# Optimization experiments

Hardware: AMD Instinct MI355X
Metric: run time of the kernel (lower is better)

## Reference

```python
import jax, jax.numpy as jnp
import numpy as np

B, T, D, H, O, E = 4, 2048, 1024, 2048, 1024, 8
EPS = 1e-12  # torch F.normalize p=1 eps


def setup_inputs() -> dict:
    key = jax.random.key(0)
    ks = jax.random.split(key, 8)
    s = lambda *dims: 1.0 / np.sqrt(dims[0])
    return {
        "x": jax.random.normal(ks[0], (B, T, D), dtype=jnp.float32),
        "num_experts_chosen": 2,
        "W_gate": jax.random.normal(ks[1], (D, E), dtype=jnp.float32) * s(D),
        "b_gate": jnp.zeros((E,), dtype=jnp.float32),
        "W1": jax.random.normal(ks[2], (E, D, H), dtype=jnp.float32) * s(D),
        "b1": jnp.zeros((E, H), dtype=jnp.float32),
        "W2": jax.random.normal(ks[3], (E, H, O), dtype=jnp.float32) * s(H),
        "b2": jnp.zeros((E, O), dtype=jnp.float32),
    }


def reference(x, num_experts_chosen, W_gate, b_gate, W1, b1, W2, b2):
    # Router: softmax over experts -> [b, t, E]
    gating = jax.nn.softmax(jnp.einsum("btd,de->bte", x, W_gate) + b_gate, axis=-1)

    # Top-k mask (scatter of ones at top-k indices), then L1 renormalize
    _, topk_idx = jax.lax.top_k(gating, num_experts_chosen)  # [b, t, k]
    mask = jax.nn.one_hot(topk_idx, E, dtype=gating.dtype).sum(axis=-2)  # [b, t, E]
    g = gating * mask
    g = g / jnp.maximum(jnp.sum(jnp.abs(g), axis=-1, keepdims=True), EPS)

    # Dense compute of ALL experts (faithful to original), eval-mode dropout = identity
    h = jax.nn.relu(jnp.einsum("btd,edh->bteh", x, W1) + b1)  # [b, t, E, H]
    eo = jnp.einsum("bteh,eho->bteo", h, W2) + b2              # [b, t, E, O]

    # Weighted combine over experts
    return jnp.einsum("bte,bteo->bto", g, eo)
```

## Files before the change

kernel.cpp:

```cpp
#include <hip/hip_runtime.h>
#include <hip/hip_bf16.h>

typedef unsigned short u16;
typedef __attribute__((ext_vector_type(8))) short short8;
typedef __attribute__((ext_vector_type(4))) float floatx4;

#define NB 4
#define NT 2048
#define ND 1024
#define NH 2048
#define NO 1024
#define NE 8
#define NTOK (NB * NT)

#define BM2 256
#define BN2 256
#define BK2 32
#define BUFU (BM2 * BK2)

__device__ __forceinline__ u16 f2bf(float f) {
  __hip_bfloat16 h = __float2bfloat16(f);
  return *reinterpret_cast<u16*>(&h);
}

__device__ __forceinline__ float bf2f(unsigned u) {
  return __uint_as_float(u << 16);
}

__device__ __forceinline__ void async16(const u16* g, u16* l) {
  __builtin_amdgcn_global_load_lds(
      (const __attribute__((address_space(1))) void*)g,
      (__attribute__((address_space(3))) void*)l, 16, 0, 0);
}

__global__ __launch_bounds__(256) void transpose_cvt(
    const float* __restrict__ in, u16* __restrict__ out, int R, int C) {
  __shared__ float tile[64][65];
  int e = blockIdx.z;
  in  += (size_t)e * R * C;
  out += (size_t)e * R * C;
  int c0 = blockIdx.x * 64, r0 = blockIdx.y * 64;
  int t = threadIdx.x;
#pragma unroll
  for (int i = 0; i < 4; ++i) {
    int idx = t + i * 256;
    int r = idx >> 4, cq = idx & 15;
    float4 v = *(const float4*)&in[(size_t)(r0 + r) * C + c0 + cq * 4];
    tile[r][cq * 4 + 0] = v.x; tile[r][cq * 4 + 1] = v.y;
    tile[r][cq * 4 + 2] = v.z; tile[r][cq * 4 + 3] = v.w;
  }
  __syncthreads();
#pragma unroll
  for (int i = 0; i < 4; ++i) {
    int idx = t + i * 256;
    int c = idx >> 4, rq = idx & 15;
    uint2 p;
    p.x = (unsigned)f2bf(tile[rq * 4 + 0][c]) | ((unsigned)f2bf(tile[rq * 4 + 1][c]) << 16);
    p.y = (unsigned)f2bf(tile[rq * 4 + 2][c]) | ((unsigned)f2bf(tile[rq * 4 + 3][c]) << 16);
    *(uint2*)&out[(size_t)(c0 + c) * R + r0 + rq * 4] = p;
  }
}

__global__ __launch_bounds__(256) void router_kernel(
    const float* __restrict__ x, const float* __restrict__ Wg,
    const float* __restrict__ bg, u16* __restrict__ xbf,
    int* __restrict__ counts, int* __restrict__ entries,
    float* __restrict__ wts) {
  __shared__ int   se0[32], se1[32];
  __shared__ float sw0[32], sw1[32];
  int t = threadIdx.x;
  int tl = t >> 3;
  int l8 = t & 7;
  int tok = blockIdx.x * 32 + tl;

  const float* xrow = x + (size_t)tok * ND;
  u16* xbrow = xbf + (size_t)tok * ND;
  float acc[8] = {};
#pragma unroll 4
  for (int i = 0; i < 32; ++i) {
    int d0 = l8 * 4 + i * 32;
    float4 xv = *(const float4*)&xrow[d0];
    uint2 p;
    p.x = (unsigned)f2bf(xv.x) | ((unsigned)f2bf(xv.y) << 16);
    p.y = (unsigned)f2bf(xv.z) | ((unsigned)f2bf(xv.w) << 16);
    *(uint2*)&xbrow[d0] = p;
    const float* wr = Wg + (size_t)d0 * NE;
#pragma unroll
    for (int j = 0; j < 4; ++j) {
      float xs = (j == 0) ? xv.x : (j == 1) ? xv.y : (j == 2) ? xv.z : xv.w;
      float4 w0 = *(const float4*)&wr[j * NE];
      float4 w1 = *(const float4*)&wr[j * NE + 4];
      acc[0] += xs * w0.x; acc[1] += xs * w0.y;
      acc[2] += xs * w0.z; acc[3] += xs * w0.w;
      acc[4] += xs * w1.x; acc[5] += xs * w1.y;
      acc[6] += xs * w1.z; acc[7] += xs * w1.w;
    }
  }
#pragma unroll
  for (int off = 4; off; off >>= 1)
#pragma unroll
    for (int k = 0; k < 8; ++k) acc[k] += __shfl_down(acc[k], off, 8);

  if (l8 == 0) {
    float best = -1e30f, second = -1e30f;
    int e0 = 0, e1 = 0;
#pragma unroll
    for (int i = 0; i < NE; ++i) {
      float L = acc[i] + bg[i];
      if (L > best) { second = best; e1 = e0; best = L; e0 = i; }
      else if (L > second) { second = L; e1 = i; }
    }
    float p1 = __expf(second - best);
    float inv = 1.f / (1.f + p1);
    se0[tl] = e0; se1[tl] = e1;
    sw0[tl] = inv; sw1[tl] = p1 * inv;
  }
  __syncthreads();

  if (t < NE) {
    int e = t;
    int c = 0;
#pragma unroll
    for (int k = 0; k < 32; ++k) c += (se0[k] == e) + (se1[k] == e);
    int pos = atomicAdd(&counts[e * 32], c);
    int base = blockIdx.x * 32;
    for (int k = 0; k < 32; ++k) {
      if (se0[k] == e) { entries[e * NTOK + pos] = (base + k) * 2;     wts[e * NTOK + pos] = sw0[k]; ++pos; }
      if (se1[k] == e) { entries[e * NTOK + pos] = (base + k) * 2 + 1; wts[e * NTOK + pos] = sw1[k]; ++pos; }
    }
  }
}

template<int KD, int NTILES, bool G2>
__global__ __launch_bounds__(512, 2) void gemm_moe(
    const u16* __restrict__ A, const u16* __restrict__ Bw,
    const float* __restrict__ bias, const int* __restrict__ counts,
    const int* __restrict__ entries, const float* __restrict__ wts,
    u16* __restrict__ out) {
  constexpr int LDO = NTILES * 256;
  constexpr int NKT = KD / BK2;

  int b = blockIdx.x;
  int e = b & 7;
  int r = b >> 3;
  int m0 = (r / NTILES) * BM2;
  int n0 = (r % NTILES) * BN2;
  int cnt = counts[e * 32];
  if (m0 >= cnt) return;
  int rem = cnt - m0; if (rem > BM2) rem = BM2;

  __shared__ __align__(16) u16 As[3 * BUFU];
  __shared__ __align__(16) u16 Bs[3 * BUFU];
  __shared__ int   ent_s[BM2];
  __shared__ float w_s[BM2];

  int t = threadIdx.x;
  if (t < BM2) {
    int src = (t < rem) ? (e * NTOK + m0 + t) : (e * NTOK);
    ent_s[t] = entries[src];
    if constexpr (G2) w_s[t] = wts[src];
  }
  __syncthreads();

  int lane = t & 63, wv = t >> 6;
  int wr = wv >> 2, wc = wv & 3;

  int rl0 = wv * 16 + (lane >> 2);
  int rl1 = rl0 + 128;
  int chS = ((lane & 3) ^ ((lane >> 3) & 3)) * 8;
  int eA0 = ent_s[rl0], eA1 = ent_s[rl1];
  size_t ra0 = G2 ? (size_t)eA0 : (size_t)(eA0 >> 1);
  size_t ra1 = G2 ? (size_t)eA1 : (size_t)(eA1 >> 1);
  const u16* pA0 = A + ra0 * KD + chS;
  const u16* pA1 = A + ra1 * KD + chS;
  const u16* Bbase = Bw + (size_t)e * LDO * KD + (size_t)n0 * KD;
  const u16* pB0 = Bbase + (size_t)rl0 * KD + chS;
  const u16* pB1 = Bbase + (size_t)rl1 * KD + chS;
  int dA0 = wv * 512;
  int dA1 = 4096 + wv * 512;

  int rA = lane & 15, q = lane >> 4;
  int pOff = rA * BK2 + ((q ^ ((rA >> 1) & 3)) * 8);
  int aOff = wr * 4096 + pOff;
  int bOff = wc * 2048 + pOff;

  floatx4 acc[8][4] = {};

  async16(pA0, As + 0 * BUFU + dA0);
  async16(pA1, As + 0 * BUFU + dA1);
  async16(pB0, Bs + 0 * BUFU + dA0);
  async16(pB1, Bs + 0 * BUFU + dA1);
  pA0 += BK2; pA1 += BK2; pB0 += BK2; pB1 += BK2;
  async16(pA0, As + 1 * BUFU + dA0);
  async16(pA1, As + 1 * BUFU + dA1);
  async16(pB0, Bs + 1 * BUFU + dA0);
  async16(pB1, Bs + 1 * BUFU + dA1);
  pA0 += BK2; pA1 += BK2; pB0 += BK2; pB1 += BK2;
  asm volatile("s_waitcnt vmcnt(4)" ::: "memory");
  __builtin_amdgcn_s_barrier();

  int rb = 0, sb = 2;
  for (int kt = 0; kt < NKT; ++kt) {
    const u16* Ab = As + rb * BUFU;
    const u16* Bb = Bs + rb * BUFU;
    u16* Ad = As + sb * BUFU;
    u16* Bd = Bs + sb * BUFU;
    short8 av[4], bv[4];

#pragma unroll
    for (int f = 0; f < 4; ++f) av[f] = *(const short8*)(Ab + aOff + f * 512);
#pragma unroll
    for (int g = 0; g < 4; ++g) bv[g] = *(const short8*)(Bb + bOff + g * 512);
    async16(pA0, Ad + dA0);
    async16(pA1, Ad + dA1);
    asm volatile("" ::: "memory");
    __builtin_amdgcn_s_barrier();
    __builtin_amdgcn_s_setprio(1);
#pragma unroll
    for (int f = 0; f < 4; ++f)
#pragma unroll
      for (int g = 0; g < 4; ++g)
        acc[f][g] = __builtin_amdgcn_mfma_f32_16x16x32_bf16(av[f], bv[g], acc[f][g], 0, 0, 0);
    __builtin_amdgcn_s_setprio(0);
    asm volatile("" ::: "memory");
    __builtin_amdgcn_s_barrier();

#pragma unroll
    for (int f = 0; f < 4; ++f) av[f] = *(const short8*)(Ab + aOff + (f + 4) * 512);
    async16(pB0, Bd + dA0);
    async16(pB1, Bd + dA1);
    asm volatile("" ::: "memory");
    __builtin_amdgcn_s_barrier();
    __builtin_amdgcn_s_setprio(1);
#pragma unroll
    for (int f = 0; f < 4; ++f)
#pragma unroll
      for (int g = 0; g < 4; ++g)
        acc[f + 4][g] = __builtin_amdgcn_mfma_f32_16x16x32_bf16(av[f], bv[g], acc[f + 4][g], 0, 0, 0);
    __builtin_amdgcn_s_setprio(0);

    if (kt + 3 < NKT) { pA0 += BK2; pA1 += BK2; pB0 += BK2; pB1 += BK2; }
    if (++rb == 3) rb = 0;
    if (++sb == 3) sb = 0;
    asm volatile("s_waitcnt vmcnt(4)" ::: "memory");
    __builtin_amdgcn_s_barrier();
  }
  asm volatile("s_waitcnt vmcnt(0)" ::: "memory");

  const float* brow = bias + (size_t)e * LDO + n0 + wc * 64;
#pragma unroll
  for (int f = 0; f < 8; ++f) {
#pragma unroll
    for (int rr = 0; rr < 4; ++rr) {
      int lm = wr * 128 + f * 16 + q * 4 + rr;
      if (lm >= rem) continue;
      int ent = ent_s[lm];
      u16* dst = out + (size_t)ent * LDO + n0 + wc * 64;
      float wgt = 1.f;
      if constexpr (G2) wgt = w_s[lm];
#pragma unroll
      for (int g = 0; g < 4; ++g) {
        int col = g * 16 + rA;
        float v = acc[f][g][rr] + brow[col];
        if constexpr (G2) v *= wgt; else v = fmaxf(v, 0.f);
        dst[col] = f2bf(v);
      }
    }
  }
}

__global__ __launch_bounds__(256) void combine_kernel(
    const u16* __restrict__ eo, float* __restrict__ out) {
  size_t idx = (size_t)blockIdx.x * 256 + threadIdx.x;
  size_t tok = idx >> 8;
  int oq = (int)(idx & 255) * 4;
  const u16* p0 = eo + (tok * 2) * NO + oq;
  const u16* p1 = p0 + NO;
  uint2 ua = *(const uint2*)p0;
  uint2 ub = *(const uint2*)p1;
  float4 o;
  o.x = bf2f(ua.x & 0xffff) + bf2f(ub.x & 0xffff);
  o.y = bf2f(ua.x >> 16)    + bf2f(ub.x >> 16);
  o.z = bf2f(ua.y & 0xffff) + bf2f(ub.y & 0xffff);
  o.w = bf2f(ua.y >> 16)    + bf2f(ub.y >> 16);
  *(float4*)&out[tok * NO + oq] = o;
}

extern "C" void kernel_launch(void* const* d_in, const int* in_sizes, int n_in,
                              void* d_out, int out_size, void* d_ws, size_t ws_size,
                              hipStream_t stream) {
  (void)in_sizes; (void)n_in; (void)out_size; (void)ws_size;
  const float* x  = (const float*)d_in[0];
  const float* Wg = (const float*)d_in[2];
  const float* bg = (const float*)d_in[3];
  const float* W1 = (const float*)d_in[4];
  const float* b1 = (const float*)d_in[5];
  const float* W2 = (const float*)d_in[6];
  const float* b2 = (const float*)d_in[7];
  float* out = (float*)d_out;

  char* ws = (char*)d_ws;
  size_t off = 0;
  int*   counts  = (int*)(ws + off);   off += NE * 32 * 4;
  int*   entries = (int*)(ws + off);   off += (size_t)NE * NTOK * 4;
  float* wts     = (float*)(ws + off); off += (size_t)NE * NTOK * 4;
  u16*   xbf     = (u16*)(ws + off);   off += (size_t)NTOK * ND * 2;
  u16*   w1t     = (u16*)(ws + off);   off += (size_t)NE * NH * ND * 2;
  u16*   w2t     = (u16*)(ws + off);   off += (size_t)NE * NO * NH * 2;
  u16*   hbuf    = (u16*)(ws + off);   off += (size_t)NTOK * 2 * NH * 2;
  u16*   eo      = w1t;

  hipMemsetAsync(counts, 0, NE * 32 * 4, stream);

  transpose_cvt<<<dim3(NH / 64, ND / 64, NE), 256, 0, stream>>>(W1, w1t, ND, NH);
  transpose_cvt<<<dim3(NO / 64, NH / 64, NE), 256, 0, stream>>>(W2, w2t, NH, NO);
  router_kernel<<<NTOK / 32, 256, 0, stream>>>(x, Wg, bg, xbf, counts, entries, wts);
  gemm_moe<ND, 8, false><<<NE * (NTOK / BM2) * 8, 512, 0, stream>>>(
      xbf, w1t, b1, counts, entries, wts, hbuf);
  gemm_moe<NH, 4, true ><<<NE * (NTOK / BM2) * 4, 512, 0, stream>>>(
      hbuf, w2t, b2, counts, entries, wts, eo);
  combine_kernel<<<(NTOK * NO / 4) / 256, 256, 0, stream>>>(eo, out);
}
```

Baseline: 531.0 us.

## Restructure MoE GEMM into 8-phase quadrant pipeline with BK=64 double buffering

Replaces the BK=32 triple-buffered main loop with BK=64 tiles in two LDS buffers, split into M/N halves. Each k-step is scheduled as four quadrant MMA phases interleaved with half-tile async loads and barriers, in the style of an 8-wave ping-pong schedule. The warp tile becomes a 2x2 grid of 64x32 sub-tiles, which changes the epilogue indexing and hoists the bias loads. The intent is to hide global-to-LDS latency and reduce barrier stalls per MFMA, at the cost of more barriers, more LDS (64KB per block) and register pressure that could hurt occupancy at 2 blocks per CU.

```diff
diff --git a/kernel.cpp b/kernel.cpp
--- a/kernel.cpp
+++ b/kernel.cpp
@@ -15,8 +15,8 @@
 
 #define BM2 256
 #define BN2 256
-#define BK2 32
-#define BUFU (BM2 * BK2)
+#define BKT 64
+#define TBUF 16384
 
 __device__ __forceinline__ u16 f2bf(float f) {
   __hip_bfloat16 h = __float2bfloat16(f);
@@ -138,7 +138,7 @@
     const int* __restrict__ entries, const float* __restrict__ wts,
     u16* __restrict__ out) {
   constexpr int LDO = NTILES * 256;
-  constexpr int NKT = KD / BK2;
+  constexpr int NI  = KD / 128;
 
   int b = blockIdx.x;
   int e = b & 7;
@@ -149,8 +149,8 @@
   if (m0 >= cnt) return;
   int rem = cnt - m0; if (rem > BM2) rem = BM2;
 
-  __shared__ __align__(16) u16 As[3 * BUFU];
-  __shared__ __align__(16) u16 Bs[3 * BUFU];
+  __shared__ __align__(16) u16 As[2 * TBUF];
+  __shared__ __align__(16) u16 Bs[2 * TBUF];
   __shared__ int   ent_s[BM2];
   __shared__ float w_s[BM2];
 
@@ -165,108 +165,146 @@
   int lane = t & 63, wv = t >> 6;
   int wr = wv >> 2, wc = wv & 3;
 
-  int rl0 = wv * 16 + (lane >> 2);
-  int rl1 = rl0 + 128;
-  int chS = ((lane & 3) ^ ((lane >> 3) & 3)) * 8;
-  int eA0 = ent_s[rl0], eA1 = ent_s[rl1];
-  size_t ra0 = G2 ? (size_t)eA0 : (size_t)(eA0 >> 1);
-  size_t ra1 = G2 ? (size_t)eA1 : (size_t)(eA1 >> 1);
-  const u16* pA0 = A + ra0 * KD + chS;
-  const u16* pA1 = A + ra1 * KD + chS;
-  const u16* Bbase = Bw + (size_t)e * LDO * KD + (size_t)n0 * KD;
-  const u16* pB0 = Bbase + (size_t)rl0 * KD + chS;
-  const u16* pB1 = Bbase + (size_t)rl1 * KD + chS;
-  int dA0 = wv * 512;
-  int dA1 = 4096 + wv * 512;
+  int srow = lane >> 3;
+  int sc   = ((lane & 7) ^ (srow & 7)) * 8;
+  const u16* aS[2][2];
+  const u16* bS[2][2];
+#pragma unroll
+  for (int h = 0; h < 2; ++h)
+#pragma unroll
+    for (int d = 0; d < 2; ++d) {
+      int rowl = h * 128 + wv * 16 + d * 8 + srow;
+      int ent = ent_s[rowl];
+      size_t ra = G2 ? (size_t)ent : (size_t)(ent >> 1);
+      aS[h][d] = A + ra * KD + sc;
+      bS[h][d] = Bw + (size_t)e * LDO * KD + (size_t)(n0 + rowl) * KD + sc;
+    }
+
+#define STAGE_A(buf, half, ko) do { int _k = (ko); if (_k >= KD) _k = 0;    \
+    async16(aS[half][0] + _k, As + (buf)*TBUF + (half)*8192 + wv*1024);      \
+    async16(aS[half][1] + _k, As + (buf)*TBUF + (half)*8192 + wv*1024 + 512);\
+  } while (0)
+#define STAGE_B(buf, half, ko) do { int _k = (ko); if (_k >= KD) _k = 0;    \
+    async16(bS[half][0] + _k, Bs + (buf)*TBUF + (half)*8192 + wv*1024);      \
+    async16(bS[half][1] + _k, Bs + (buf)*TBUF + (half)*8192 + wv*1024 + 512);\
+  } while (0)
 
   int rA = lane & 15, q = lane >> 4;
-  int pOff = rA * BK2 + ((q ^ ((rA >> 1) & 3)) * 8);
-  int aOff = wr * 4096 + pOff;
-  int bOff = wc * 2048 + pOff;
-
-  floatx4 acc[8][4] = {};
-
-  async16(pA0, As + 0 * BUFU + dA0);
-  async16(pA1, As + 0 * BUFU + dA1);
-  async16(pB0, Bs + 0 * BUFU + dA0);
-  async16(pB1, Bs + 0 * BUFU + dA1);
-  pA0 += BK2; pA1 += BK2; pB0 += BK2; pB1 += BK2;
-  async16(pA0, As + 1 * BUFU + dA0);
-  async16(pA1, As + 1 * BUFU + dA1);
-  async16(pB0, Bs + 1 * BUFU + dA0);
-  async16(pB1, Bs + 1 * BUFU + dA1);
-  pA0 += BK2; pA1 += BK2; pB0 += BK2; pB1 += BK2;
-  asm volatile("s_waitcnt vmcnt(4)" ::: "memory");
-  __builtin_amdgcn_s_barrier();
-
-  int rb = 0, sb = 2;
-  for (int kt = 0; kt < NKT; ++kt) {
-    const u16* Ab = As + rb * BUFU;
-    const u16* Bb = Bs + rb * BUFU;
-    u16* Ad = As + sb * BUFU;
-    u16* Bd = Bs + sb * BUFU;
-    short8 av[4], bv[4];
-
-#pragma unroll
-    for (int f = 0; f < 4; ++f) av[f] = *(const short8*)(Ab + aOff + f * 512);
-#pragma unroll
-    for (int g = 0; g < 4; ++g) bv[g] = *(const short8*)(Bb + bOff + g * 512);
-    async16(pA0, Ad + dA0);
-    async16(pA1, Ad + dA1);
-    asm volatile("" ::: "memory");
-    __builtin_amdgcn_s_barrier();
-    __builtin_amdgcn_s_setprio(1);
+  int aRow = (wr * 64 + rA) * 64;
+  int bRow = (wc * 32 + rA) * 64;
+  int ch0 = ((q) ^ (rA & 7)) * 8;
+  int ch1 = ((4 + q) ^ (rA & 7)) * 8;
+
+  short8 a[2][4];
+  short8 bb[2][2][2];
+  floatx4 acc[2][2][4][2] = {};
+
+#define LDA(mh, buf) do {                                                   \
+    const u16* _p = As + (buf)*TBUF + (mh)*8192 + aRow;                      \
+    _Pragma("unroll") for (int f = 0; f < 4; ++f) {                          \
+      a[0][f] = *(const short8*)(_p + f*1024 + ch0);                         \
+      a[1][f] = *(const short8*)(_p + f*1024 + ch1); } } while (0)
+#define LDB(nh, buf) do {                                                   \
+    const u16* _p = Bs + (buf)*TBUF + (nh)*8192 + bRow;                      \
+    _Pragma("unroll") for (int nf = 0; nf < 2; ++nf) {                       \
+      bb[nh][0][nf] = *(const short8*)(_p + nf*1024 + ch0);                  \
+      bb[nh][1][nf] = *(const short8*)(_p + nf*1024 + ch1); } } while (0)
+#define MM(mh, nh)                                                           \
+    __builtin_amdgcn_s_setprio(1);                                           \
+    _Pragma("unroll") for (int kk = 0; kk < 2; ++kk)                         \
+    _Pragma("unroll") for (int f = 0; f < 4; ++f)                            \
+    _Pragma("unroll") for (int nf = 0; nf < 2; ++nf)                         \
+      acc[mh][nh][f][nf] = __builtin_amdgcn_mfma_f32_16x16x32_bf16(          \
+          a[kk][f], bb[nh][kk][nf], acc[mh][nh][f][nf], 0, 0, 0);            \
+    __builtin_amdgcn_s_setprio(0);
+#define FEN asm volatile("" ::: "memory")
+#define BAR __builtin_amdgcn_s_barrier()
+#define VM6 asm volatile("s_waitcnt vmcnt(6)" ::: "memory")
+
+  STAGE_A(0, 0, 0);  STAGE_B(0, 0, 0);  STAGE_A(0, 1, 0);  STAGE_B(0, 1, 0);
+  STAGE_A(1, 0, 64); STAGE_B(1, 0, 64); STAGE_A(1, 1, 64);
+  VM6; FEN; BAR;
+
+  for (int it = 0; it < NI; ++it) {
+    int kb = it * 128;
+    LDA(0, 0); LDB(0, 0);
+    STAGE_B(1, 1, 64 + kb);
+    FEN; BAR;
+    MM(0, 0);
+    FEN; BAR;
+    LDB(1, 0);
+    STAGE_A(0, 0, 128 + kb);
+    FEN; BAR;
+    MM(0, 1);
+    FEN; BAR;
+    LDA(1, 0);
+    STAGE_B(0, 0, 128 + kb);
+    FEN; BAR;
+    MM(1, 0);
+    FEN; BAR;
+    STAGE_A(0, 1, 128 + kb);
+    FEN; BAR;
+    MM(1, 1);
+    VM6; FEN; BAR;
+    LDA(0, 1); LDB(0, 1);
+    STAGE_B(0, 1, 128 + kb);
+    FEN; BAR;
+    MM(0, 0);
+    FEN; BAR;
+    LDB(1, 1);
+    STAGE_A(1, 0, 192 + kb);
+    FEN; BAR;
+    MM(0, 1);
+    FEN; BAR;
+    LDA(1, 1);
+    STAGE_B(1, 0, 192 + kb);
+    FEN; BAR;
+    MM(1, 0);
+    FEN; BAR;
+    STAGE_A(1, 1, 192 + kb);
+    FEN; BAR;
+    MM(1, 1);
+    VM6; FEN; BAR;
+  }
+  asm volatile("s_waitcnt vmcnt(0)" ::: "memory");
+
+  float bcol[2][2];
+#pragma unroll
+  for (int nh = 0; nh < 2; ++nh)
+#pragma unroll
+    for (int nf = 0; nf < 2; ++nf)
+      bcol[nh][nf] = bias[e * LDO + n0 + wc * 32 + nh * 128 + nf * 16 + rA];
+
+#pragma unroll
+  for (int mh = 0; mh < 2; ++mh)
 #pragma unroll
     for (int f = 0; f < 4; ++f)
 #pragma unroll
-      for (int g = 0; g < 4; ++g)
-        acc[f][g] = __builtin_amdgcn_mfma_f32_16x16x32_bf16(av[f], bv[g], acc[f][g], 0, 0, 0);
-    __builtin_amdgcn_s_setprio(0);
-    asm volatile("" ::: "memory");
-    __builtin_amdgcn_s_barrier();
-
-#pragma unroll
-    for (int f = 0; f < 4; ++f) av[f] = *(const short8*)(Ab + aOff + (f + 4) * 512);
-    async16(pB0, Bd + dA0);
-    async16(pB1, Bd + dA1);
-    asm volatile("" ::: "memory");
-    __builtin_amdgcn_s_barrier();
-    __builtin_amdgcn_s_setprio(1);
-#pragma unroll
-    for (int f = 0; f < 4; ++f)
-#pragma unroll
-      for (int g = 0; g < 4; ++g)
-        acc[f + 4][g] = __builtin_amdgcn_mfma_f32_16x16x32_bf16(av[f], bv[g], acc[f + 4][g], 0, 0, 0);
-    __builtin_amdgcn_s_setprio(0);
-
-    if (kt + 3 < NKT) { pA0 += BK2; pA1 += BK2; pB0 += BK2; pB1 += BK2; }
-    if (++rb == 3) rb = 0;
-    if (++sb == 3) sb = 0;
-    asm volatile("s_waitcnt vmcnt(4)" ::: "memory");
-    __builtin_amdgcn_s_barrier();
-  }
-  asm volatile("s_waitcnt vmcnt(0)" ::: "memory");
-
-  const float* brow = bias + (size_t)e * LDO + n0 + wc * 64;
-#pragma unroll
-  for (int f = 0; f < 8; ++f) {
-#pragma unroll
-    for (int rr = 0; rr < 4; ++rr) {
-      int lm = wr * 128 + f * 16 + q * 4 + rr;
-      if (lm >= rem) continue;
-      int ent = ent_s[lm];
-      u16* dst = out + (size_t)ent * LDO + n0 + wc * 64;
-      float wgt = 1.f;
-      if constexpr (G2) wgt = w_s[lm];
-#pragma unroll
-      for (int g = 0; g < 4; ++g) {
-        int col = g * 16 + rA;
-        float v = acc[f][g][rr] + brow[col];
-        if constexpr (G2) v *= wgt; else v = fmaxf(v, 0.f);
-        dst[col] = f2bf(v);
+      for (int rr = 0; rr < 4; ++rr) {
+        int lm = wr * 64 + mh * 128 + f * 16 + q * 4 + rr;
+        if (lm >= rem) continue;
+        int ent = ent_s[lm];
+        float wgt = 1.f;
+        if constexpr (G2) wgt = w_s[lm];
+        u16* dst = out + (size_t)ent * LDO + n0;
+#pragma unroll
+        for (int nh = 0; nh < 2; ++nh)
+#pragma unroll
+          for (int nf = 0; nf < 2; ++nf) {
+            int col = wc * 32 + nh * 128 + nf * 16 + rA;
+            float v = acc[mh][nh][f][nf][rr] + bcol[nh][nf];
+            if constexpr (G2) v *= wgt; else v = fmaxf(v, 0.f);
+            dst[col] = f2bf(v);
+          }
       }
-    }
-  }
+#undef STAGE_A
+#undef STAGE_B
+#undef LDA
+#undef LDB
+#undef MM
+#undef FEN
+#undef BAR
+#undef VM6
 }
 
 __global__ __launch_bounds__(256) void combine_kernel(
```

Measured after the change: 481.3 us. -9.4%, faster.

## Replace pipelined 256x256 MoE GEMM with simple 128x128 persistent-stride kernels

Applied to the files above, without the earlier changes.

Swaps the templated triple-buffered 256x256 tile GEMM (512 threads, async prefetch, setprio) for two separate 128x128-tile kernels with 256 threads. Each block now covers a fixed grid of 16 M-slots per expert and strides over M tiles in a loop. Loads are single-buffered and synchronous, with barriers around each K step. Smaller tiles may balance uneven expert counts better, but the change gives up software pipelining and the higher arithmetic intensity of the larger tiles.

```diff
diff --git a/kernel.cpp b/kernel.cpp
--- a/kernel.cpp
+++ b/kernel.cpp
@@ -13,10 +13,9 @@
 #define NE 8
 #define NTOK (NB * NT)
 
-#define BM2 256
-#define BN2 256
-#define BK2 32
-#define BUFU (BM2 * BK2)
+#define BM 128
+#define BN 128
+#define BK 32
 
 __device__ __forceinline__ u16 f2bf(float f) {
   __hip_bfloat16 h = __float2bfloat16(f);
@@ -131,141 +130,176 @@
   }
 }
 
-template<int KD, int NTILES, bool G2>
-__global__ __launch_bounds__(512, 2) void gemm_moe(
-    const u16* __restrict__ A, const u16* __restrict__ Bw,
-    const float* __restrict__ bias, const int* __restrict__ counts,
-    const int* __restrict__ entries, const float* __restrict__ wts,
-    u16* __restrict__ out) {
-  constexpr int LDO = NTILES * 256;
-  constexpr int NKT = KD / BK2;
-
+__global__ __launch_bounds__(256) void gemm1_kernel(
+    const u16* __restrict__ xbf, const u16* __restrict__ w1t,
+    const float* __restrict__ b1, const int* __restrict__ counts,
+    const int* __restrict__ entries, u16* __restrict__ hbuf) {
   int b = blockIdx.x;
   int e = b & 7;
   int r = b >> 3;
-  int m0 = (r / NTILES) * BM2;
-  int n0 = (r % NTILES) * BN2;
+  int mIdx = r >> 4;
+  int n0 = (r & 15) * BN;
   int cnt = counts[e * 32];
-  if (m0 >= cnt) return;
-  int rem = cnt - m0; if (rem > BM2) rem = BM2;
-
-  __shared__ __align__(16) u16 As[3 * BUFU];
-  __shared__ __align__(16) u16 Bs[3 * BUFU];
-  __shared__ int   ent_s[BM2];
-  __shared__ float w_s[BM2];
+
+  __shared__ u16 As[BM * BK];
+  __shared__ u16 Bs[BN * BK];
+  __shared__ int ent_s[BM];
 
   int t = threadIdx.x;
-  if (t < BM2) {
-    int src = (t < rem) ? (e * NTOK + m0 + t) : (e * NTOK);
-    ent_s[t] = entries[src];
-    if constexpr (G2) w_s[t] = wts[src];
-  }
-  __syncthreads();
-
   int lane = t & 63, wv = t >> 6;
-  int wr = wv >> 2, wc = wv & 3;
-
-  int rl0 = wv * 16 + (lane >> 2);
-  int rl1 = rl0 + 128;
-  int chS = ((lane & 3) ^ ((lane >> 3) & 3)) * 8;
-  int eA0 = ent_s[rl0], eA1 = ent_s[rl1];
-  size_t ra0 = G2 ? (size_t)eA0 : (size_t)(eA0 >> 1);
-  size_t ra1 = G2 ? (size_t)eA1 : (size_t)(eA1 >> 1);
-  const u16* pA0 = A + ra0 * KD + chS;
-  const u16* pA1 = A + ra1 * KD + chS;
-  const u16* Bbase = Bw + (size_t)e * LDO * KD + (size_t)n0 * KD;
-  const u16* pB0 = Bbase + (size_t)rl0 * KD + chS;
-  const u16* pB1 = Bbase + (size_t)rl1 * KD + chS;
-  int dA0 = wv * 512;
-  int dA1 = 4096 + wv * 512;
-
-  int rA = lane & 15, q = lane >> 4;
-  int pOff = rA * BK2 + ((q ^ ((rA >> 1) & 3)) * 8);
-  int aOff = wr * 4096 + pOff;
-  int bOff = wc * 2048 + pOff;
-
-  floatx4 acc[8][4] = {};
-
-  async16(pA0, As + 0 * BUFU + dA0);
-  async16(pA1, As + 0 * BUFU + dA1);
-  async16(pB0, Bs + 0 * BUFU + dA0);
-  async16(pB1, Bs + 0 * BUFU + dA1);
-  pA0 += BK2; pA1 += BK2; pB0 += BK2; pB1 += BK2;
-  async16(pA0, As + 1 * BUFU + dA0);
-  async16(pA1, As + 1 * BUFU + dA1);
-  async16(pB0, Bs + 1 * BUFU + dA0);
-  async16(pB1, Bs + 1 * BUFU + dA1);
-  pA0 += BK2; pA1 += BK2; pB0 += BK2; pB1 += BK2;
-  asm volatile("s_waitcnt vmcnt(4)" ::: "memory");
-  __builtin_amdgcn_s_barrier();
-
-  int rb = 0, sb = 2;
-  for (int kt = 0; kt < NKT; ++kt) {
-    const u16* Ab = As + rb * BUFU;
-    const u16* Bb = Bs + rb * BUFU;
-    u16* Ad = As + sb * BUFU;
-    u16* Bd = Bs + sb * BUFU;
-    short8 av[4], bv[4];
-
-#pragma unroll
-    for (int f = 0; f < 4; ++f) av[f] = *(const short8*)(Ab + aOff + f * 512);
-#pragma unroll
-    for (int g = 0; g < 4; ++g) bv[g] = *(const short8*)(Bb + bOff + g * 512);
-    async16(pA0, Ad + dA0);
-    async16(pA1, Ad + dA1);
-    asm volatile("" ::: "memory");
-    __builtin_amdgcn_s_barrier();
-    __builtin_amdgcn_s_setprio(1);
-#pragma unroll
-    for (int f = 0; f < 4; ++f)
-#pragma unroll
-      for (int g = 0; g < 4; ++g)
-        acc[f][g] = __builtin_amdgcn_mfma_f32_16x16x32_bf16(av[f], bv[g], acc[f][g], 0, 0, 0);
-    __builtin_amdgcn_s_setprio(0);
-    asm volatile("" ::: "memory");
-    __builtin_amdgcn_s_barrier();
-
-#pragma unroll
-    for (int f = 0; f < 4; ++f) av[f] = *(const short8*)(Ab + aOff + (f + 4) * 512);
-    async16(pB0, Bd + dA0);
-    async16(pB1, Bd + dA1);
-    asm volatile("" ::: "memory");
-    __builtin_amdgcn_s_barrier();
-    __builtin_amdgcn_s_setprio(1);
-#pragma unroll
-    for (int f = 0; f < 4; ++f)
-#pragma unroll
-      for (int g = 0; g < 4; ++g)
-        acc[f + 4][g] = __builtin_amdgcn_mfma_f32_16x16x32_bf16(av[f], bv[g], acc[f + 4][g], 0, 0, 0);
-    __builtin_amdgcn_s_setprio(0);
-
-    if (kt + 3 < NKT) { pA0 += BK2; pA1 += BK2; pB0 += BK2; pB1 += BK2; }
-    if (++rb == 3) rb = 0;
-    if (++sb == 3) sb = 0;
-    asm volatile("s_waitcnt vmcnt(4)" ::: "memory");
-    __builtin_amdgcn_s_barrier();
-  }
-  asm volatile("s_waitcnt vmcnt(0)" ::: "memory");
-
-  const float* brow = bias + (size_t)e * LDO + n0 + wc * 64;
-#pragma unroll
-  for (int f = 0; f < 8; ++f) {
-#pragma unroll
-    for (int rr = 0; rr < 4; ++rr) {
-      int lm = wr * 128 + f * 16 + q * 4 + rr;
-      if (lm >= rem) continue;
-      int ent = ent_s[lm];
-      u16* dst = out + (size_t)ent * LDO + n0 + wc * 64;
-      float wgt = 1.f;
-      if constexpr (G2) wgt = w_s[lm];
-#pragma unroll
-      for (int g = 0; g < 4; ++g) {
-        int col = g * 16 + rA;
-        float v = acc[f][g][rr] + brow[col];
-        if constexpr (G2) v *= wgt; else v = fmaxf(v, 0.f);
-        dst[col] = f2bf(v);
+  int rl0 = wv * 32 + (lane >> 2);
+  int rl1 = rl0 + 16;
+  int pg = (((lane & 3) ^ ((rl0 >> 1) & 3))) * 8;
+  const u16* Bbase = w1t + (size_t)e * NH * ND + (size_t)n0 * ND;
+  const u16* gB0 = Bbase + (size_t)rl0 * ND + pg;
+  const u16* gB1 = Bbase + (size_t)rl1 * ND + pg;
+  u16* lA0 = As + (wv * 32) * BK;
+  u16* lA1 = As + (wv * 32 + 16) * BK;
+  u16* lB0 = Bs + (wv * 32) * BK;
+  u16* lB1 = Bs + (wv * 32 + 16) * BK;
+
+  int waveM = (wv >> 1) * 64, waveN = (wv & 1) * 64;
+  int rA = lane & 15, quad = lane >> 4;
+  int cR = (quad ^ ((rA >> 1) & 3)) * 8;
+  const short8* aP[4]; const short8* bP[4];
+#pragma unroll
+  for (int i = 0; i < 4; ++i) {
+    aP[i] = (const short8*)&As[(waveM + i * 16 + rA) * BK + cR];
+    bP[i] = (const short8*)&Bs[(waveN + i * 16 + rA) * BK + cR];
+  }
+
+  for (int m0 = mIdx * BM; m0 < cnt; m0 += 16 * BM) {
+    int rem = cnt - m0; if (rem > BM) rem = BM;
+    if (t < BM) ent_s[t] = (t < rem) ? entries[e * NTOK + m0 + t] : entries[e * NTOK];
+    __syncthreads();
+
+    const u16* gA0 = xbf + (size_t)(ent_s[rl0] >> 1) * ND + pg;
+    const u16* gA1 = xbf + (size_t)(ent_s[rl1] >> 1) * ND + pg;
+
+    floatx4 acc[4][4] = {};
+    for (int k0 = 0; k0 < ND; k0 += BK) {
+      async16(gA0 + k0, lA0);
+      async16(gA1 + k0, lA1);
+      async16(gB0 + k0, lB0);
+      async16(gB1 + k0, lB1);
+      __syncthreads();
+      short8 a[4], bb[4];
+#pragma unroll
+      for (int i = 0; i < 4; ++i) { a[i] = *aP[i]; bb[i] = *bP[i]; }
+#pragma unroll
+      for (int i = 0; i < 4; ++i)
+#pragma unroll
+        for (int j = 0; j < 4; ++j)
+          acc[i][j] = __builtin_amdgcn_mfma_f32_16x16x32_bf16(a[i], bb[j], acc[i][j], 0, 0, 0);
+      __syncthreads();
+    }
+
+#pragma unroll
+    for (int i = 0; i < 4; ++i)
+#pragma unroll
+      for (int rr = 0; rr < 4; ++rr) {
+        int lm = waveM + i * 16 + quad * 4 + rr;
+        if (lm >= rem) continue;
+        int ent = ent_s[lm];
+        u16* dst = hbuf + (size_t)ent * NH + n0;
+#pragma unroll
+        for (int j = 0; j < 4; ++j) {
+          int col = waveN + j * 16 + rA;
+          float v = acc[i][j][rr] + b1[e * NH + n0 + col];
+          dst[col] = f2bf(fmaxf(v, 0.f));
+        }
       }
-    }
+    __syncthreads();
+  }
+}
+
+__global__ __launch_bounds__(256) void gemm2_kernel(
+    const u16* __restrict__ hbuf, const u16* __restrict__ w2t,
+    const float* __restrict__ b2, const int* __restrict__ counts,
+    const int* __restrict__ entries, const float* __restrict__ wts,
+    u16* __restrict__ eo) {
+  int b = blockIdx.x;
+  int e = b & 7;
+  int r = b >> 3;
+  int mIdx = r >> 3;
+  int n0 = (r & 7) * BN;
+  int cnt = counts[e * 32];
+
+  __shared__ u16 As[BM * BK];
+  __shared__ u16 Bs[BN * BK];
+  __shared__ int ent_s[BM];
+  __shared__ float w_s[BM];
+
+  int t = threadIdx.x;
+  int lane = t & 63, wv = t >> 6;
+  int rl0 = wv * 32 + (lane >> 2);
+  int rl1 = rl0 + 16;
+  int pg = (((lane & 3) ^ ((rl0 >> 1) & 3))) * 8;
+  const u16* Bbase = w2t + (size_t)e * NO * NH + (size_t)n0 * NH;
+  const u16* gB0 = Bbase + (size_t)rl0 * NH + pg;
+  const u16* gB1 = Bbase + (size_t)rl1 * NH + pg;
+  u16* lA0 = As + (wv * 32) * BK;
+  u16* lA1 = As + (wv * 32 + 16) * BK;
+  u16* lB0 = Bs + (wv * 32) * BK;
+  u16* lB1 = Bs + (wv * 32 + 16) * BK;
+
+  int waveM = (wv >> 1) * 64, waveN = (wv & 1) * 64;
+  int rA = lane & 15, quad = lane >> 4;
+  int cR = (quad ^ ((rA >> 1) & 3)) * 8;
+  const short8* aP[4]; const short8* bP[4];
+#pragma unroll
+  for (int i = 0; i < 4; ++i) {
+    aP[i] = (const short8*)&As[(waveM + i * 16 + rA) * BK + cR];
+    bP[i] = (const short8*)&Bs[(waveN + i * 16 + rA) * BK + cR];
+  }
+
+  for (int m0 = mIdx * BM; m0 < cnt; m0 += 16 * BM) {
+    int rem = cnt - m0; if (rem > BM) rem = BM;
+    if (t < BM) {
+      int src = (t < rem) ? (e * NTOK + m0 + t) : (e * NTOK);
+      ent_s[t] = entries[src];
+      w_s[t] = wts[src];
+    }
+    __syncthreads();
+
+    const u16* gA0 = hbuf + (size_t)ent_s[rl0] * NH + pg;
+    const u16* gA1 = hbuf + (size_t)ent_s[rl1] * NH + pg;
+
+    floatx4 acc[4][4] = {};
+    for (int k0 = 0; k0 < NH; k0 += BK) {
+      async16(gA0 + k0, lA0);
+      async16(gA1 + k0, lA1);
+      async16(gB0 + k0, lB0);
+      async16(gB1 + k0, lB1);
+      __syncthreads();
+      short8 a[4], bb[4];
+#pragma unroll
+      for (int i = 0; i < 4; ++i) { a[i] = *aP[i]; bb[i] = *bP[i]; }
+#pragma unroll
+      for (int i = 0; i < 4; ++i)
+#pragma unroll
+        for (int j = 0; j < 4; ++j)
+          acc[i][j] = __builtin_amdgcn_mfma_f32_16x16x32_bf16(a[i], bb[j], acc[i][j], 0, 0, 0);
+      __syncthreads();
+    }
+
+#pragma unroll
+    for (int i = 0; i < 4; ++i)
+#pragma unroll
+      for (int rr = 0; rr < 4; ++rr) {
+        int lm = waveM + i * 16 + quad * 4 + rr;
+        if (lm >= rem) continue;
+        int ent = ent_s[lm];
+        float w = w_s[lm];
+        u16* dst = eo + (size_t)ent * NO + n0;
+#pragma unroll
+        for (int j = 0; j < 4; ++j) {
+          int col = waveN + j * 16 + rA;
+          float v = (acc[i][j][rr] + b2[e * NO + n0 + col]) * w;
+          dst[col] = f2bf(v);
+        }
+      }
+    __syncthreads();
   }
 }
 
@@ -315,9 +349,7 @@
   transpose_cvt<<<dim3(NH / 64, ND / 64, NE), 256, 0, stream>>>(W1, w1t, ND, NH);
   transpose_cvt<<<dim3(NO / 64, NH / 64, NE), 256, 0, stream>>>(W2, w2t, NH, NO);
   router_kernel<<<NTOK / 32, 256, 0, stream>>>(x, Wg, bg, xbf, counts, entries, wts);
-  gemm_moe<ND, 8, false><<<NE * (NTOK / BM2) * 8, 512, 0, stream>>>(
-      xbf, w1t, b1, counts, entries, wts, hbuf);
-  gemm_moe<NH, 4, true ><<<NE * (NTOK / BM2) * 4, 512, 0, stream>>>(
-      hbuf, w2t, b2, counts, entries, wts, eo);
+  gemm1_kernel<<<NE * 16 * (NH / BN), 256, 0, stream>>>(xbf, w1t, b1, counts, entries, hbuf);
+  gemm2_kernel<<<NE * 16 * (NO / BN), 256, 0, stream>>>(hbuf, w2t, b2, counts, entries, wts, eo);
   combine_kernel<<<(NTOK * NO / 4) / 256, 256, 0, stream>>>(eo, out);
 }
```

After: 502.9 us. 1.06x faster.
